# Kernel tuning notes

Measured on AMD Instinct MI355X. Metric: run time of the kernel, lower is better.

The kernel has to match this reference:

```python
import jax, jax.numpy as jnp
import numpy as np

L = 4        # transformer layers
C = 128      # width
CIN = 2      # obs channels
BS = 9       # boardsize
S = BS * BS  # attention sequence length (81)
EPS = 1e-5


def setup_inputs() -> dict:
    key = jax.random.key(0)
    ks = jax.random.split(key, 6)

    def w(k, shape, scale):
        return jax.random.normal(k, shape, dtype=jnp.float32) * scale

    return {
        "x": jax.random.normal(ks[0], (4, 32, BS, BS, CIN), dtype=jnp.float32),
        # input projection (stored as [in, out] so y = x @ W + b)
        "in_w": w(ks[1], (CIN, C), CIN ** -0.5),
        "in_b": jnp.zeros((C,), jnp.float32),
        # per-layer LayerNorm affine params
        "ln_g": jnp.ones((L, C), jnp.float32),
        "ln_b": jnp.zeros((L, C), jnp.float32),
        # per-layer qkv and output linears
        "qkv_w": w(ks[2], (L, C, 3 * C), C ** -0.5),
        "qkv_b": jnp.zeros((L, 3 * C), jnp.float32),
        "full_w": w(ks[3], (L, C, C), C ** -0.5),
        "full_b": jnp.zeros((L, C), jnp.float32),
        # final projection to 4 channels
        "out_w": w(ks[4], (C, 4), C ** -0.5),
        "out_b": jnp.zeros((4,), jnp.float32),
    }


def _layernorm(x, g, b):
    mu = jnp.mean(x, axis=-1, keepdims=True)
    var = jnp.var(x, axis=-1, keepdims=True)
    return (x - mu) * jax.lax.rsqrt(var + EPS) * g + b


def reference(x, in_w, in_b, ln_g, ln_b, qkv_w, qkv_b, full_w, full_b, out_w, out_b):
    T, B, H, W, _ = x.shape
    h = x @ in_w + in_b  # [T,B,H,W,C]
    for i in range(L):
        n = _layernorm(h.reshape(T * B, S, C), ln_g[i], ln_b[i])  # [TB,S,C]
        qkv = n @ qkv_w[i] + qkv_b[i]
        q, k, v = jnp.split(qkv, 3, axis=-1)  # each [TB,S,C]
        # per-channel attention: no reduction over C before softmax
        sim = jnp.einsum('bqc,bkc->bqkc', q, k)        # [TB,S,S,C]
        attn = jax.nn.softmax(sim, axis=2)             # softmax over k per channel
        att = jnp.einsum('bqkc,bkc->bqc', attn, v)     # [TB,S,C]
        att = att.reshape(T, B, H, W, C)
        y = jax.nn.relu(att @ full_w[i] + full_b[i])
        h = h + y
    return h @ out_w + out_b  # [T,B,H,W,4]
```

## Files before the change

kernel.cpp:

```cpp
#include <hip/hip_runtime.h>

#define NQKV_ 384
#define MAGIC_ 0x5CA1AB1E
#define HSTRIDE 140
#define QSTRIDE 65
#define KSTRIDE 66

typedef __bf16 bf;
typedef __attribute__((ext_vector_type(4))) __bf16 bf16x4;
typedef __attribute__((ext_vector_type(8))) __bf16 bf16x8;
typedef __attribute__((ext_vector_type(4))) float f32x4;

__device__ __forceinline__ float fast_exp2(float x) {
#if __has_builtin(__builtin_amdgcn_exp2f)
  return __builtin_amdgcn_exp2f(x);
#else
  return exp2f(x);
#endif
}
__device__ __forceinline__ float fast_rcp(float x) {
#if __has_builtin(__builtin_amdgcn_rcpf)
  return __builtin_amdgcn_rcpf(x);
#else
  return 1.0f / x;
#endif
}

__global__ __launch_bounds__(256) void k_prep_w(const float* __restrict__ qkv_w,
                                                const float* __restrict__ full_w,
                                                bf* __restrict__ wq, bf* __restrict__ wf) {
  __shared__ float tile[128][17];
  const int blk = blockIdx.x, tid = threadIdx.x;
  const float* src;
  bf* dst;
  int ldn;
  if (blk < 96) {
    int layer = blk / 24, t = blk % 24;
    src = qkv_w + (size_t)layer * 128 * NQKV_ + t * 16;
    dst = wq + ((size_t)blk << 11);
    ldn = NQKV_;
  } else {
    int b2 = blk - 96;
    src = full_w + (size_t)(b2 >> 3) * 128 * 128 + (b2 & 7) * 16;
    dst = wf + ((size_t)b2 << 11);
    ldn = 128;
  }
#pragma unroll
  for (int pass = 0; pass < 2; ++pass) {
    int k = (tid >> 2) + pass * 64;
    int c4 = (tid & 3) * 4;
    float4 f = *(const float4*)(src + (size_t)k * ldn + c4);
    tile[k][c4 + 0] = f.x; tile[k][c4 + 1] = f.y;
    tile[k][c4 + 2] = f.z; tile[k][c4 + 3] = f.w;
  }
  __syncthreads();
  int s = tid >> 6, lane = tid & 63;
  int k0 = s * 32 + ((lane >> 4) << 3), n16 = lane & 15;
  bf16x8 v;
#pragma unroll
  for (int j = 0; j < 8; ++j) v[j] = (bf)tile[k0 + j][n16];
  *(bf16x8*)(dst + tid * 8) = v;
}

__global__ __launch_bounds__(1024)
__attribute__((amdgpu_waves_per_eu(4, 4))) void k_net(
    const float* __restrict__ x, const float* __restrict__ in_w,
    const float* __restrict__ in_b, const float* __restrict__ ln_g,
    const float* __restrict__ ln_b, const float* __restrict__ qkv_b,
    const float* __restrict__ full_b, const float* __restrict__ out_w,
    const float* __restrict__ out_b, const bf* __restrict__ wq,
    const bf* __restrict__ wf, bf* __restrict__ attg,
    int* __restrict__ flags, float* __restrict__ out) {
  __shared__ __align__(16) float h_s[81 * HSTRIDE];
  __shared__ __align__(16) bf afrag[96 * 128];
  __shared__ float q_s[81 * QSTRIDE];
  __shared__ float kvf[81 * KSTRIDE * 2];

  const int tid = threadIdx.x;
  const int bidx = blockIdx.x;
  const int b = bidx & 127, half = bidx >> 7, c0 = half * 64;
  const int wave = tid >> 6, lane = tid & 63, l15 = lane & 15, quad = lane >> 4;
  const float log2e = 1.4426950408889634f;

  bf* ag_own = attg + (size_t)(b * 2 + half) * 6144;
  const bf* ag_peer = attg + (size_t)(b * 2 + (1 - half)) * 6144;

  {
    const float* xb = x + (size_t)b * 162;
    for (int i = tid; i < 81 * 128; i += 1024) {
      int p = i >> 7, cc = i & 127;
      h_s[p * HSTRIDE + cc] = xb[p * 2] * in_w[cc] + xb[p * 2 + 1] * in_w[128 + cc] + in_b[cc];
    }
  }
  __syncthreads();

  for (int layer = 0; layer < 4; ++layer) {
    const bf* wqL = wq + (size_t)layer * 24 * 2048;
    const bf* wfL = wf + (size_t)layer * 8 * 2048;

    {
      const float* lg = ln_g + layer * 128;
      const float* lb = ln_b + layer * 128;
      int row = tid >> 3, g8 = tid & 7;
      if (row < 81) {
        const float* hr = h_s + row * HSTRIDE;
        float vals[16];
        float sum = 0.f, ssq = 0.f;
#pragma unroll
        for (int it = 0; it < 4; ++it) {
          float4 f = *(const float4*)(hr + g8 * 4 + it * 32);
          vals[it * 4 + 0] = f.x; vals[it * 4 + 1] = f.y;
          vals[it * 4 + 2] = f.z; vals[it * 4 + 3] = f.w;
          sum += f.x + f.y + f.z + f.w;
          ssq += f.x * f.x + f.y * f.y + f.z * f.z + f.w * f.w;
        }
#pragma unroll
        for (int off = 1; off < 8; off <<= 1) {
          sum += __shfl_xor(sum, off);
          ssq += __shfl_xor(ssq, off);
        }
        float mu = sum * (1.f / 128.f);
        float rs = rsqrtf(ssq * (1.f / 128.f) - mu * mu + 1e-5f);
        int mt = row >> 4, m = row & 15;
        int lgp = g8 >> 1, j0 = (g8 & 1) * 4;
#pragma unroll
        for (int it = 0; it < 4; ++it) {
          int cc = g8 * 4 + it * 32;
          float4 gg = *(const float4*)(lg + cc);
          float4 bb = *(const float4*)(lb + cc);
          bf16x4 nv;
          nv[0] = (bf)((vals[it * 4 + 0] - mu) * rs * gg.x + bb.x);
          nv[1] = (bf)((vals[it * 4 + 1] - mu) * rs * gg.y + bb.y);
          nv[2] = (bf)((vals[it * 4 + 2] - mu) * rs * gg.z + bb.z);
          nv[3] = (bf)((vals[it * 4 + 3] - mu) * rs * gg.w + bb.w);
          *(bf16x4*)(afrag + (((mt * 4 + it) * 64 + (lgp * 16 + m)) << 3) + j0) = nv;
        }
      }
    }
    __syncthreads();

    {
      f32x4 acc[5] = {};
#pragma unroll
      for (int i = 0; i < 5; ++i) {
        int tau = wave + 16 * i;
        if (tau < 72) {
          int Mt = tau / 12, Nt = tau % 12;
          int sec = Nt >> 2, off = Nt & 3;
          int tg = sec * 8 + half * 4 + off;
#pragma unroll
          for (int s = 0; s < 4; ++s) {
            bf16x8 a = *(const bf16x8*)(afrag + (((Mt * 4 + s) * 64 + lane) << 3));
            bf16x8 bb = *(const bf16x8*)(wqL + ((tg * 4 + s) * 512 + lane * 8));
            acc[i] = __builtin_amdgcn_mfma_f32_16x16x32_bf16(a, bb, acc[i], 0, 0, 0);
          }
        }
      }
      const float* qb = qkv_b + layer * NQKV_;
#pragma unroll
      for (int i = 0; i < 5; ++i) {
        int tau = wave + 16 * i;
        if (tau < 72) {
          int Mt = tau / 12, Nt = tau % 12;
          int sec = Nt >> 2, off = Nt & 3;
          int cl = off * 16 + l15;
          float bias = qb[sec * 128 + c0 + cl];
          int Rb = Mt * 16 + quad * 4;
#pragma unroll
          for (int r = 0; r < 4; ++r) {
            int R = Rb + r;
            if (R < 81) {
              float vv = acc[i][r] + bias;
              if (sec == 0)      q_s[R * QSTRIDE + cl] = vv * log2e;
              else if (sec == 1) kvf[(R * KSTRIDE + cl) * 2] = vv;
              else               kvf[(R * KSTRIDE + cl) * 2 + 1] = vv;
            }
          }
        }
      }
    }
    __syncthreads();

    {
      int c = tid & 63, qs = wave;
      int cc = c0 + c;
      unsigned int* agc = (unsigned int*)ag_own;
      unsigned int* afu = (unsigned int*)afrag;

      float xq[6], Na[6], Da[6];
#pragma unroll
      for (int j = 0; j < 5; ++j) {
        xq[j] = q_s[(qs + 16 * j) * QSTRIDE + c];
        Na[j] = 0.f; Da[j] = 0.f;
      }
      xq[5] = 0.f; Na[5] = 0.f; Da[5] = 0.f;
      if (qs == 0) {
        xq[5] = q_s[80 * QSTRIDE + c];
#pragma unroll 3
        for (int kk = 0; kk < 81; ++kk) {
          float2 A = *(const float2*)(kvf + (kk * KSTRIDE + c) * 2);
#pragma unroll
          for (int j = 0; j < 6; ++j) {
            float e = fast_exp2(xq[j] * A.x);
            Da[j] += e; Na[j] = __builtin_fmaf(e, A.y, Na[j]);
          }
        }
      } else {
#pragma unroll 3
        for (int kk = 0; kk < 81; ++kk) {
          float2 A = *(const float2*)(kvf + (kk * KSTRIDE + c) * 2);
#pragma unroll
          for (int j = 0; j < 5; ++j) {
            float e = fast_exp2(xq[j] * A.x);
            Da[j] += e; Na[j] = __builtin_fmaf(e, A.y, Na[j]);
          }
        }
      }
#pragma unroll
      for (int j = 0; j < 6; ++j) {
        if (j == 5 && qs != 0) break;
        int qq = qs + 16 * j;
        bf bv = (bf)(Na[j] * fast_rcp(Da[j]));
        unsigned int u = (unsigned int)__builtin_bit_cast(unsigned short, bv);
        unsigned int un = ((unsigned int)__shfl_xor((int)u, 1)) & 0xffffu;
        if ((c & 1) == 0) {
          unsigned int packed = u | (un << 16);
          int qc = (cc >> 3) & 3, jc = cc & 7, m = qq & 15, Mt = qq >> 4;
          int fragu = (((Mt * 4 + (cc >> 5)) * 512) + qc * 128 + m * 8 + jc) >> 1;
          afu[fragu] = packed;
          int compu = ((Mt * 1024) + ((cc >> 5) & 1) * 512 + qc * 128 + m * 8 + jc) >> 1;
          __hip_atomic_store(agc + compu, packed, __ATOMIC_RELAXED,
                             __HIP_MEMORY_SCOPE_AGENT);
        }
      }
    }
    __syncthreads();

    if (tid == 0) {
      __hip_atomic_store(&flags[bidx * 4 + layer], MAGIC_, __ATOMIC_RELEASE,
                         __HIP_MEMORY_SCOPE_AGENT);
    }
    f32x4 acc[3] = {};
    {
      int sbase = half * 2;
#pragma unroll
      for (int i = 0; i < 3; ++i) {
        int tau = wave + 16 * i;
        int Mt = tau >> 3, Nt = tau & 7;
#pragma unroll
        for (int ss = 0; ss < 2; ++ss) {
          int s = sbase + ss;
          bf16x8 a = *(const bf16x8*)(afrag + (((Mt * 4 + s) * 64 + lane) << 3));
          bf16x8 bb = *(const bf16x8*)(wfL + ((Nt * 4 + s) * 512 + lane * 8));
          acc[i] = __builtin_amdgcn_mfma_f32_16x16x32_bf16(a, bb, acc[i], 0, 0, 0);
        }
      }
    }
    if (tid == 0) {
      int peer = (bidx ^ 128) * 4 + layer;
      long guard = 0;
      while (__hip_atomic_load(&flags[peer], __ATOMIC_RELAXED,
                               __HIP_MEMORY_SCOPE_AGENT) != MAGIC_) {
        __builtin_amdgcn_s_sleep(2);
        if (++guard > (1L << 27)) break;
      }
    }
    __syncthreads();

    {
      const unsigned long long* peer8 = (const unsigned long long*)ag_peer;
      unsigned long long* af8 = (unsigned long long*)afrag;
      int sbaseG = 2 - half * 2;
      for (int t = tid; t < 1536; t += 1024) {
        int j = t & 1, ln2 = (t >> 1) & 63, ss = (t >> 7) & 1, Mt = t >> 8;
        unsigned long long v = __hip_atomic_load(peer8 + t, __ATOMIC_RELAXED,
                                                 __HIP_MEMORY_SCOPE_AGENT);
        af8[((Mt * 4 + sbaseG + ss) * 64 + ln2) * 2 + j] = v;
      }
    }
    __syncthreads();

    {
      int pbase = 2 - half * 2;
#pragma unroll
      for (int i = 0; i < 3; ++i) {
        int tau = wave + 16 * i;
        int Mt = tau >> 3, Nt = tau & 7;
#pragma unroll
        for (int ss = 0; ss < 2; ++ss) {
          int s = pbase + ss;
          bf16x8 a = *(const bf16x8*)(afrag + (((Mt * 4 + s) * 64 + lane) << 3));
          bf16x8 bb = *(const bf16x8*)(wfL + ((Nt * 4 + s) * 512 + lane * 8));
          acc[i] = __builtin_amdgcn_mfma_f32_16x16x32_bf16(a, bb, acc[i], 0, 0, 0);
        }
      }
      const float* fb = full_b + layer * 128;
#pragma unroll
      for (int i = 0; i < 3; ++i) {
        int tau = wave + 16 * i;
        int Mt = tau >> 3, Nt = tau & 7;
        int col = Nt * 16 + l15;
        float bias = fb[col];
        int Rb = Mt * 16 + quad * 4;
#pragma unroll
        for (int r = 0; r < 4; ++r) {
          int R = Rb + r;
          if (R < 81) h_s[R * HSTRIDE + col] += fmaxf(acc[i][r] + bias, 0.f);
        }
      }
    }
    __syncthreads();
  }

  if (half == 0) {
    int row = tid >> 3, g8 = tid & 7;
    if (row < 81) {
      const float* hr = h_s + row * HSTRIDE;
      float o0 = 0.f, o1 = 0.f, o2 = 0.f, o3 = 0.f;
#pragma unroll
      for (int it = 0; it < 4; ++it) {
        int cc = g8 * 4 + it * 32;
        float4 f = *(const float4*)(hr + cc);
        float4 wA = *(const float4*)(out_w + (cc + 0) * 4);
        float4 wB = *(const float4*)(out_w + (cc + 1) * 4);
        float4 wC = *(const float4*)(out_w + (cc + 2) * 4);
        float4 wD = *(const float4*)(out_w + (cc + 3) * 4);
        o0 += f.x * wA.x + f.y * wB.x + f.z * wC.x + f.w * wD.x;
        o1 += f.x * wA.y + f.y * wB.y + f.z * wC.y + f.w * wD.y;
        o2 += f.x * wA.z + f.y * wB.z + f.z * wC.z + f.w * wD.z;
        o3 += f.x * wA.w + f.y * wB.w + f.z * wC.w + f.w * wD.w;
      }
#pragma unroll
      for (int off = 1; off < 8; off <<= 1) {
        o0 += __shfl_xor(o0, off); o1 += __shfl_xor(o1, off);
        o2 += __shfl_xor(o2, off); o3 += __shfl_xor(o3, off);
      }
      if (g8 == 0) {
        *(float4*)(out + ((size_t)b * 81 + row) * 4) =
            make_float4(o0 + out_b[0], o1 + out_b[1], o2 + out_b[2], o3 + out_b[3]);
      }
    }
  }
}

extern "C" void kernel_launch(void* const* d_in, const int* in_sizes, int n_in,
                              void* d_out, int out_size, void* d_ws, size_t ws_size,
                              hipStream_t stream) {
  const float* x      = (const float*)d_in[0];
  const float* in_w   = (const float*)d_in[1];
  const float* in_b   = (const float*)d_in[2];
  const float* ln_g   = (const float*)d_in[3];
  const float* ln_b   = (const float*)d_in[4];
  const float* qkv_w  = (const float*)d_in[5];
  const float* qkv_b  = (const float*)d_in[6];
  const float* full_w = (const float*)d_in[7];
  const float* full_b = (const float*)d_in[8];
  const float* out_w  = (const float*)d_in[9];
  const float* out_b  = (const float*)d_in[10];

  bf* wq     = (bf*)d_ws;
  bf* wf     = wq + 196608;
  bf* attg   = wf + 65536;
  int* flags = (int*)(attg + 1572864);
  float* out = (float*)d_out;

  k_prep_w<<<128, 256, 0, stream>>>(qkv_w, full_w, wq, wf);
  k_net<<<256, 1024, 0, stream>>>(x, in_w, in_b, ln_g, ln_b, qkv_b, full_b,
                                  out_w, out_b, wq, wf, attg, flags, out);
}
```

Baseline: 188.3 us.

## Fuse weight-prep kernel into main kernel with cross-block flag handshake

Drops the separate k_prep_w launch. Each block of k_net now converts a slice of the qkv/full weights into the bf16 MFMA fragment layout and then publishes a readiness flag. Before its first layer's QKV GEMM, each block spins until all 256 prep flags are set. This removes one kernel launch and its dependency gap, but it relies on all blocks being co-resident and adds a grid-wide spin wait. It also weakens the per-layer flag store from release to relaxed ordering and uses only a workgroup-scope acquire fence after the wait, so it risks memory-ordering problems.

```diff
diff --git a/kernel.cpp b/kernel.cpp
--- a/kernel.cpp
+++ b/kernel.cpp
@@ -26,51 +26,17 @@
 #endif
 }
 
-__global__ __launch_bounds__(256) void k_prep_w(const float* __restrict__ qkv_w,
-                                                const float* __restrict__ full_w,
-                                                bf* __restrict__ wq, bf* __restrict__ wf) {
-  __shared__ float tile[128][17];
-  const int blk = blockIdx.x, tid = threadIdx.x;
-  const float* src;
-  bf* dst;
-  int ldn;
-  if (blk < 96) {
-    int layer = blk / 24, t = blk % 24;
-    src = qkv_w + (size_t)layer * 128 * NQKV_ + t * 16;
-    dst = wq + ((size_t)blk << 11);
-    ldn = NQKV_;
-  } else {
-    int b2 = blk - 96;
-    src = full_w + (size_t)(b2 >> 3) * 128 * 128 + (b2 & 7) * 16;
-    dst = wf + ((size_t)b2 << 11);
-    ldn = 128;
-  }
-#pragma unroll
-  for (int pass = 0; pass < 2; ++pass) {
-    int k = (tid >> 2) + pass * 64;
-    int c4 = (tid & 3) * 4;
-    float4 f = *(const float4*)(src + (size_t)k * ldn + c4);
-    tile[k][c4 + 0] = f.x; tile[k][c4 + 1] = f.y;
-    tile[k][c4 + 2] = f.z; tile[k][c4 + 3] = f.w;
-  }
-  __syncthreads();
-  int s = tid >> 6, lane = tid & 63;
-  int k0 = s * 32 + ((lane >> 4) << 3), n16 = lane & 15;
-  bf16x8 v;
-#pragma unroll
-  for (int j = 0; j < 8; ++j) v[j] = (bf)tile[k0 + j][n16];
-  *(bf16x8*)(dst + tid * 8) = v;
-}
-
 __global__ __launch_bounds__(1024)
 __attribute__((amdgpu_waves_per_eu(4, 4))) void k_net(
     const float* __restrict__ x, const float* __restrict__ in_w,
     const float* __restrict__ in_b, const float* __restrict__ ln_g,
-    const float* __restrict__ ln_b, const float* __restrict__ qkv_b,
+    const float* __restrict__ ln_b, const float* __restrict__ qkv_w,
+    const float* __restrict__ qkv_b, const float* __restrict__ full_w,
     const float* __restrict__ full_b, const float* __restrict__ out_w,
-    const float* __restrict__ out_b, const bf* __restrict__ wq,
-    const bf* __restrict__ wf, bf* __restrict__ attg,
-    int* __restrict__ flags, float* __restrict__ out) {
+    const float* __restrict__ out_b, bf* __restrict__ wq,
+    bf* __restrict__ wf, bf* __restrict__ attg,
+    int* __restrict__ flags, int* __restrict__ pflags,
+    float* __restrict__ out) {
   __shared__ __align__(16) float h_s[81 * HSTRIDE];
   __shared__ __align__(16) bf afrag[96 * 128];
   __shared__ float q_s[81 * QSTRIDE];
@@ -84,6 +50,41 @@
 
   bf* ag_own = attg + (size_t)(b * 2 + half) * 6144;
   const bf* ag_peer = attg + (size_t)(b * 2 + (1 - half)) * 6144;
+
+  {
+    int p = bidx & 127, hp = bidx >> 7;
+    int pl = p >> 5, u = p & 31;
+    const float* srcw;
+    bf* dstt;
+    int ldn, n0;
+    if (u < 24) {
+      srcw = qkv_w + (size_t)pl * 128 * NQKV_;
+      dstt = wq + ((size_t)(pl * 24 + u) << 11);
+      ldn = NQKV_; n0 = u * 16;
+    } else {
+      srcw = full_w + (size_t)pl * 128 * 128;
+      dstt = wf + ((size_t)(pl * 8 + (u - 24)) << 11);
+      ldn = 128; n0 = (u - 24) * 16;
+    }
+    if (tid < 256) {
+      int g = hp * 1024 + tid * 4;
+      int s = g >> 9, l = (g >> 3) & 63, j0 = g & 7;
+      int kb = s * 32 + ((l >> 4) << 3) + j0;
+      int n = n0 + (l & 15);
+      unsigned long long pk = 0;
+#pragma unroll
+      for (int jj = 0; jj < 4; ++jj) {
+        bf v = (bf)srcw[(size_t)(kb + jj) * ldn + n];
+        pk |= (unsigned long long)__builtin_bit_cast(unsigned short, v) << (16 * jj);
+      }
+      __hip_atomic_store((unsigned long long*)(dstt + g), pk, __ATOMIC_RELAXED,
+                         __HIP_MEMORY_SCOPE_AGENT);
+    }
+    __syncthreads();
+    if (tid == 0)
+      __hip_atomic_store(&pflags[p * 2 + hp], MAGIC_, __ATOMIC_RELAXED,
+                         __HIP_MEMORY_SCOPE_AGENT);
+  }
 
   {
     const float* xb = x + (size_t)b * 162;
@@ -138,6 +139,24 @@
       }
     }
     __syncthreads();
+
+    if (layer == 0) {
+      if (wave == 0) {
+        long guard = 0;
+        for (;;) {
+          int ok = 1;
+#pragma unroll
+          for (int t = 0; t < 4; ++t)
+            ok &= (__hip_atomic_load(&pflags[t * 64 + lane], __ATOMIC_RELAXED,
+                                     __HIP_MEMORY_SCOPE_AGENT) == MAGIC_);
+          if (__all(ok)) break;
+          __builtin_amdgcn_s_sleep(2);
+          if (++guard > (1L << 24)) break;
+        }
+      }
+      __syncthreads();
+      __builtin_amdgcn_fence(__ATOMIC_ACQUIRE, "workgroup");
+    }
 
     {
       f32x4 acc[5] = {};
@@ -237,7 +256,7 @@
     __syncthreads();
 
     if (tid == 0) {
-      __hip_atomic_store(&flags[bidx * 4 + layer], MAGIC_, __ATOMIC_RELEASE,
+      __hip_atomic_store(&flags[bidx * 4 + layer], MAGIC_, __ATOMIC_RELAXED,
                          __HIP_MEMORY_SCOPE_AGENT);
     }
     f32x4 acc[3] = {};
@@ -358,13 +377,14 @@
   const float* out_w  = (const float*)d_in[9];
   const float* out_b  = (const float*)d_in[10];
 
-  bf* wq     = (bf*)d_ws;
-  bf* wf     = wq + 196608;
-  bf* attg   = wf + 65536;
-  int* flags = (int*)(attg + 1572864);
-  float* out = (float*)d_out;
-
-  k_prep_w<<<128, 256, 0, stream>>>(qkv_w, full_w, wq, wf);
-  k_net<<<256, 1024, 0, stream>>>(x, in_w, in_b, ln_g, ln_b, qkv_b, full_b,
-                                  out_w, out_b, wq, wf, attg, flags, out);
+  bf* wq      = (bf*)d_ws;
+  bf* wf      = wq + 196608;
+  bf* attg    = wf + 65536;
+  int* flags  = (int*)(attg + 1572864);
+  int* pflags = flags + 1024;
+  float* out  = (float*)d_out;
+
+  k_net<<<256, 1024, 0, stream>>>(x, in_w, in_b, ln_g, ln_b, qkv_w, qkv_b,
+                                  full_w, full_b, out_w, out_b, wq, wf, attg,
+                                  flags, pflags, out);
 }
```

Measured after the change: 177.3 us. 5.8% less time.
